# Kernel tuning notes

Hardware: AMD Instinct MI355X
Metric: run time of the kernel (lower is better)

The kernel has to match this reference:

```python
import jax, jax.numpy as jnp
import numpy as np

B, W, F, H = 2048, 64, 128, 128


def setup_inputs() -> dict:
    key = jax.random.key(0)
    ks = jax.random.split(key, 23)
    n = lambda k, shape: jax.random.normal(k, shape, dtype=jnp.float32) * 0.05
    return dict(
        X=jax.random.normal(ks[0], (B, W, F), dtype=jnp.float32),
        # InputAttention: linear1 (W+2H -> W), linear2 (W -> 1)
        ia_W1=n(ks[1], (W, W + 2 * H)), ia_b1=n(ks[2], (W,)),
        ia_W2=n(ks[3], (1, W)), ia_b2=n(ks[4], (1,)),
        # encoder LSTMCell(F, H)
        enc_Wih=n(ks[5], (4 * H, F)), enc_Whh=n(ks[6], (4 * H, H)),
        enc_bih=n(ks[7], (4 * H,)), enc_bhh=n(ks[8], (4 * H,)),
        # TemporalAttention: linear1 (3H -> H), linear2 (H -> 1)
        ta_W1=n(ks[9], (H, 3 * H)), ta_b1=n(ks[10], (H,)),
        ta_W2=n(ks[11], (1, H)), ta_b2=n(ks[12], (1,)),
        # decoder LSTMCell(1, H)
        dec_Wih=n(ks[13], (4 * H, 1)), dec_Whh=n(ks[14], (4 * H, H)),
        dec_bih=n(ks[15], (4 * H,)), dec_bhh=n(ks[16], (4 * H,)),
        # output heads
        l1_W=n(ks[17], (1, 1 + H)), l1_b=n(ks[18], (1,)),
        l2_W=n(ks[19], (H, 2 * H)), l2_b=n(ks[20], (H,)),
        l3_W=n(ks[21], (1, H)), l3_b=n(ks[22], (1,)),
    )


def _lstm_cell(x, h, c, Wih, Whh, bih, bhh):
    g = x @ Wih.T + bih + h @ Whh.T + bhh
    i, f, gg, o = jnp.split(g, 4, axis=-1)
    c_new = jax.nn.sigmoid(f) * c + jax.nn.sigmoid(i) * jnp.tanh(gg)
    h_new = jax.nn.sigmoid(o) * jnp.tanh(c_new)
    return h_new, c_new


def reference(X, ia_W1, ia_b1, ia_W2, ia_b2,
              enc_Wih, enc_Whh, enc_bih, enc_bhh,
              ta_W1, ta_b1, ta_W2, ta_b2,
              dec_Wih, dec_Whh, dec_bih, dec_bhh,
              l1_W, l1_b, l2_W, l2_b, l3_W, l3_b):
    Bsz, Wlen, Fdim = X.shape
    Hdim = enc_Whh.shape[1]
    Xf = jnp.transpose(X, (2, 0, 1))  # [F, B, W] (feature-major view for input attention)

    # ---- encoder with input attention ----
    def enc_step(carry, xt):  # xt: [B, F]
        h, c = carry
        hr = jnp.broadcast_to(h[None], (Fdim, Bsz, Hdim))
        cr = jnp.broadcast_to(c[None], (Fdim, Bsz, Hdim))
        u = jnp.tanh(jnp.concatenate([Xf, hr, cr], axis=-1) @ ia_W1.T + ia_b1)  # [F,B,W]
        e = u @ ia_W2.T + ia_b2                                                  # [F,B,1]
        alpha = jax.nn.softmax(e, axis=0)[..., 0].T                              # [B,F]
        h_new, c_new = _lstm_cell(alpha * xt, h, c, enc_Wih, enc_Whh, enc_bih, enc_bhh)
        return (h_new, c_new), h_new

    z = jnp.zeros((Bsz, Hdim), dtype=X.dtype)
    (_, _), Hs = jax.lax.scan(enc_step, (z, z), jnp.transpose(X, (1, 0, 2)))  # Hs: [W,B,H]
    # dropout: eval mode (identity)

    # ---- decoder with temporal attention ----
    def dec_step(carry, _):
        d, ds, out = carry
        dr = jnp.broadcast_to(d[None], Hs.shape)
        dsr = jnp.broadcast_to(ds[None], Hs.shape)
        v = jnp.tanh(jnp.concatenate([Hs, dr, dsr], axis=-1) @ ta_W1.T + ta_b1)  # [W,B,H]
        l = v @ ta_W2.T + ta_b2                                                   # [W,B,1]
        beta = jax.nn.softmax(l, axis=0)
        ct = jnp.sum(beta * Hs, axis=0)                                           # [B,H]
        yt = jnp.concatenate([out, ct], axis=-1) @ l1_W.T + l1_b                  # [B,1]
        d_new, ds_new = _lstm_cell(yt, d, ds, dec_Wih, dec_Whh, dec_bih, dec_bhh)
        o = jnp.concatenate([ct, d_new], axis=-1) @ l2_W.T + l2_b
        out_new = jax.nn.sigmoid(o @ l3_W.T + l3_b)                               # [B,1]
        return (d_new, ds_new, out_new), None

    out0 = jnp.zeros((Bsz, 1), dtype=X.dtype)
    (_, _, output), _ = jax.lax.scan(dec_step, (z, z, out0), None, length=Wlen)
    return output
```

## Files before the change

kernel.cpp:

```cpp
#include <hip/hip_runtime.h>
#include <hip/hip_fp16.h>
#include <stdint.h>

typedef unsigned int uint;
typedef unsigned short ushort;

#define NB 2048
#define NW 64
#define NF 128
#define NH 128

typedef __attribute__((ext_vector_type(8))) short s8v;
typedef __attribute__((ext_vector_type(8))) _Float16 h8v;
typedef __attribute__((ext_vector_type(4))) float f4v;

#define MFMA16(a, b, c) __builtin_amdgcn_mfma_f32_16x16x32_bf16((a), (b), (c), 0, 0, 0)
#define MFMAH(a, b, c)  __builtin_amdgcn_mfma_f32_16x16x32_f16((a), (b), (c), 0, 0, 0)

union H8 { h8v v; __half2 h2[4]; uint4 u4; ushort us[8]; };

__device__ __forceinline__ float bfl(uint u){ return __uint_as_float(u << 16); }
__device__ __forceinline__ float bfh(uint u){ return __uint_as_float(u & 0xffff0000u); }
__device__ __forceinline__ ushort f2bf(float f){
  uint u = __float_as_uint(f);
  u += 0x7fffu + ((u >> 16) & 1u);
  return (ushort)(u >> 16);
}
__device__ __forceinline__ float bf2f(ushort s){ return __uint_as_float(((uint)s) << 16); }

__device__ __forceinline__ float fast_tanh(float x){
  float e = __expf(x + x);
  return 1.f - 2.f * __builtin_amdgcn_rcpf(e + 1.f);
}
__device__ __forceinline__ float fast_sig(float x){
  return __builtin_amdgcn_rcpf(1.f + __expf(-x));
}
__device__ __forceinline__ ushort expo_h(float x){
  return __half_as_ushort(__float2half(__expf(x + x)));
}

__device__ __forceinline__ s8v packW(const float* p){
  s8v r;
  #pragma unroll
  for (int i = 0; i < 8; ++i) r[i] = (short)f2bf(p[i]);
  return r;
}

__global__ __launch_bounds__(256) void k_upre(const float* __restrict__ X,
                                              const float* __restrict__ iaW1,
                                              ushort* __restrict__ Eenc){
  __shared__ __align__(16) float sXT[128*68];
  const int tid = threadIdx.x, lane = tid & 63, wave = tid >> 6, g = lane >> 4;
  int b = blockIdx.x;
  const float* Xb = X + (size_t)b*NW*NF;
  for (int i = tid; i < NW*NF; i += 256){
    int j = i >> 7, f = i & 127;
    sXT[f*68 + j] = Xb[i];
  }
  s8v bw[2];
  {
    int w = wave*16 + (lane & 15);
    #pragma unroll
    for (int kb = 0; kb < 2; ++kb) bw[kb] = packW(iaW1 + w*320 + kb*32 + g*8);
  }
  __syncthreads();
  ushort* outb = Eenc + (size_t)b*NF*NW;
  int w = wave*16 + (lane & 15);
  #pragma unroll
  for (int mt = 0; mt < 8; ++mt){
    int f = mt*16 + (lane & 15);
    f4v acc = {0.f,0.f,0.f,0.f};
    #pragma unroll
    for (int kb = 0; kb < 2; ++kb){
      const float* p = &sXT[f*68 + kb*32 + g*8];
      s8v a;
      #pragma unroll
      for (int i = 0; i < 8; ++i) a[i] = (short)f2bf(p[i]);
      acc = MFMA16(a, bw[kb], acc);
    }
    int fr = mt*16 + g*4;
    #pragma unroll
    for (int j = 0; j < 4; ++j) outb[(fr + j)*64 + w] = expo_h(acc[j]);
  }
}

__global__ __launch_bounds__(256) void k_vpre(const ushort* __restrict__ Hsb,
                                              const float* __restrict__ taW1,
                                              ushort* __restrict__ Edec,
                                              ushort* __restrict__ HsT){
  __shared__ __align__(16) ushort sH[64*136];
  const int tid = threadIdx.x, lane = tid & 63, wave = tid >> 6, g = lane >> 4;
  int b = blockIdx.x;
  const ushort* Hb = Hsb + (size_t)b*NW*NH;
  for (int i = tid; i < 1024; i += 256){
    int w = i >> 4, c = i & 15;
    *(uint4*)&sH[w*136 + c*8] = *(const uint4*)(Hb + i*8);
  }
  s8v bw[2][4];
  #pragma unroll
  for (int nt = 0; nt < 2; ++nt){
    int h = wave*32 + nt*16 + (lane & 15);
    #pragma unroll
    for (int kb = 0; kb < 4; ++kb)
      bw[nt][kb] = packW(taW1 + h*384 + kb*32 + g*8);
  }
  __syncthreads();
  ushort* ho = HsT + (size_t)b*NH*NW;
  for (int k = 0; k < 32; ++k){
    int i2 = tid + 256*k;
    int h = i2 >> 6, w2 = i2 & 63;
    ho[i2] = sH[w2*136 + h];
  }
  ushort* outb = Edec + (size_t)b*NW*NH;
  #pragma unroll
  for (int mt = 0; mt < 4; ++mt){
    s8v af[4];
    #pragma unroll
    for (int kb = 0; kb < 4; ++kb)
      af[kb] = *(const s8v*)&sH[(mt*16 + (lane&15))*136 + kb*32 + g*8];
    #pragma unroll
    for (int nt = 0; nt < 2; ++nt){
      f4v acc = {0.f,0.f,0.f,0.f};
      #pragma unroll
      for (int kb = 0; kb < 4; ++kb) acc = MFMA16(af[kb], bw[nt][kb], acc);
      int h = wave*32 + nt*16 + (lane&15);
      int wr = mt*16 + g*4;
      #pragma unroll
      for (int j = 0; j < 4; ++j) outb[(wr + j)*128 + h] = expo_h(acc[j]);
    }
  }
}

__global__ __launch_bounds__(512, 2) void k_enc(
    const float* __restrict__ X, const float* __restrict__ iaW1,
    const float* __restrict__ iab1, const float* __restrict__ iaW2,
    const float* __restrict__ encWih, const float* __restrict__ encWhh,
    const float* __restrict__ encbih, const float* __restrict__ encbhh,
    const ushort* __restrict__ Eenc, ushort* __restrict__ Hsb){
  __shared__ __align__(16) ushort sUp[65536];
  __shared__ __align__(16) ushort sAB[16*264];
  __shared__ __align__(16) ushort uhc_h[8*64];
  __shared__ __align__(16) float  c_s[8*128];
  __shared__ __align__(16) float  bias_s[512];
  __shared__ __align__(16) float  xrow[8*128];

  const int tid = threadIdx.x, lane = tid & 63, wave = tid >> 6, g = lane >> 4;
  const int bbase = blockIdx.x * 8;

  for (int i = tid; i < 16*264; i += 512) sAB[i] = 0;
  for (int i = tid; i < 1024; i += 512) c_s[i] = 0.f;
  bias_s[tid] = encbih[tid] + encbhh[tid];
  {
    const ushort* up0 = Eenc + (size_t)bbase*NF*NW;
    #pragma unroll
    for (int k = 0; k < 16; ++k){
      int c = tid + k*512;
      int f = (c >> 3) & 127, s = c & 7;
      uint4 v = *(const uint4*)(up0 + (size_t)c*8);
      *(uint4*)((char*)sUp + (c>>3)*128 + ((s ^ (f & 7)) << 4)) = v;
    }
  }
  s8v bwC[4][8];
  #pragma unroll
  for (int gg = 0; gg < 4; ++gg){
    int j = gg*128 + wave*16 + (lane & 15);
    #pragma unroll
    for (int kc = 0; kc < 8; ++kc){
      const float* p = (kc < 4) ? (encWih + j*128 + kc*32) : (encWhh + j*128 + (kc-4)*32);
      bwC[gg][kc] = packW(p + g*8);
    }
  }
  s8v bwA[8];
  if (wave < 4){
    int n = wave*16 + (lane & 15);
    #pragma unroll
    for (int kc = 0; kc < 8; ++kc){
      int col = (kc < 4) ? (192 + kc*32) : (64 + (kc-4)*32);
      bwA[kc] = packW(iaW1 + n*320 + col + g*8);
    }
  }
  H8 w2f[2];
  #pragma unroll
  for (int kb = 0; kb < 2; ++kb)
    #pragma unroll
    for (int i = 0; i < 8; ++i)
      w2f[kb].v[i] = (_Float16)iaW2[kb*32 + g*8 + i];
  __syncthreads();

  for (int t = 0; t < NW; ++t){
    {
      const float* Xr = X + ((size_t)(bbase + wave)*NW + t)*NF;
      xrow[wave*128 + lane] = Xr[lane];
      xrow[wave*128 + 64 + lane] = Xr[64 + lane];
    }
    s8v aT[8];
    #pragma unroll
    for (int kc = 0; kc < 8; ++kc)
      aT[kc] = *(const s8v*)((const char*)sAB + (lane&15)*528 + kc*64 + g*16);
    if (wave < 4){
      f4v acc = {0.f,0.f,0.f,0.f};
      #pragma unroll
      for (int kc = 0; kc < 8; ++kc) acc = MFMA16(aT[kc], bwA[kc], acc);
      if (lane < 32){
        int n = wave*16 + (lane & 15);
        float b1v = iab1[n];
        int mb = g*4;
        #pragma unroll
        for (int j = 0; j < 4; ++j) uhc_h[(mb+j)*64 + n] = expo_h(acc[j] + b1v);
      }
    }
    __syncthreads();

    {
      int bb = wave;
      const char* Eb = (const char*)sUp + bb*16384;
      H8 sv[2];
      #pragma unroll
      for (int kb = 0; kb < 2; ++kb)
        sv[kb].u4 = *(const uint4*)((const char*)uhc_h + bb*128 + kb*64 + g*16);
      __half2 one2 = __float2half2_rn(1.f);
      f4v Mc[8];
      #pragma unroll
      for (int ft = 0; ft < 8; ++ft){
        int f = ft*16 + (lane & 15);
        const char* rowp = Eb + f*128;
        f4v acc = {0.f,0.f,0.f,0.f};
        #pragma unroll
        for (int kb = 0; kb < 2; ++kb){
          H8 e, a;
          e.v = *(const h8v*)(rowp + (((kb*4 + g) ^ (f & 7)) << 4));
          #pragma unroll
          for (int q = 0; q < 4; ++q) a.h2[q] = h2rcp(__hfma2(e.h2[q], sv[kb].h2[q], one2));
          acc = MFMAH(a.v, w2f[kb].v, acc);
        }
        Mc[ft] = acc;
      }
      float mn = Mc[0][0];
      #pragma unroll
      for (int ft = 0; ft < 8; ++ft)
        #pragma unroll
        for (int r = 0; r < 4; ++r) mn = fminf(mn, Mc[ft][r]);
      mn = fminf(mn, __shfl_xor(mn, 16, 64));
      mn = fminf(mn, __shfl_xor(mn, 32, 64));
      float xs[8][4]; float ssum = 0.f;
      #pragma unroll
      for (int ft = 0; ft < 8; ++ft)
        #pragma unroll
        for (int r = 0; r < 4; ++r){ float x = __expf(2.f*(mn - Mc[ft][r])); xs[ft][r] = x; ssum += x; }
      ssum += __shfl_xor(ssum, 16, 64);
      ssum += __shfl_xor(ssum, 32, 64);
      float inv = __builtin_amdgcn_rcpf(ssum);
      if ((lane & 15) == 0){
        #pragma unroll
        for (int ft = 0; ft < 8; ++ft){
          int f0 = ft*16 + g*4;
          float4 Xv = *(const float4*)&xrow[bb*128 + f0];
          uint lo = (uint)f2bf(xs[ft][0]*inv*Xv.x) | ((uint)f2bf(xs[ft][1]*inv*Xv.y) << 16);
          uint hi = (uint)f2bf(xs[ft][2]*inv*Xv.z) | ((uint)f2bf(xs[ft][3]*inv*Xv.w) << 16);
          *(uint2*)((char*)sAB + bb*528 + f0*2) = make_uint2(lo, hi);
        }
      }
    }
    __syncthreads();

    s8v aX[4];
    #pragma unroll
    for (int kc = 0; kc < 4; ++kc)
      aX[kc] = *(const s8v*)((const char*)sAB + (lane&15)*528 + kc*64 + g*16);
    __syncthreads();

    {
      f4v acc[4];
      #pragma unroll
      for (int gg = 0; gg < 4; ++gg) acc[gg] = (f4v){0.f,0.f,0.f,0.f};
      #pragma unroll
      for (int kc = 0; kc < 8; ++kc){
        s8v af = (kc < 4) ? aX[kc] : aT[kc];
        #pragma unroll
        for (int gg = 0; gg < 4; ++gg) acc[gg] = MFMA16(af, bwC[gg][kc], acc[gg]);
      }
      if (lane < 32){
        int n16 = wave*16 + (lane & 15);
        int mb = g*4;
        float bi = bias_s[n16], bf_ = bias_s[128+n16], bg = bias_s[256+n16], bo = bias_s[384+n16];
        #pragma unroll
        for (int j = 0; j < 4; ++j){
          int m = mb + j;
          float gi = acc[0][j] + bi;
          float gf = acc[1][j] + bf_;
          float gg2 = acc[2][j] + bg;
          float go = acc[3][j] + bo;
          float cold = c_s[m*128 + n16];
          float cn = fast_sig(gf)*cold + fast_sig(gi)*fast_tanh(gg2);
          float hn = fast_sig(go)*fast_tanh(cn);
          c_s[m*128 + n16] = cn;
          sAB[m*264 + n16] = f2bf(cn);
          sAB[m*264 + 128 + n16] = f2bf(hn);
          Hsb[((size_t)(bbase + m)*NW + t)*NH + n16] = f2bf(hn);
        }
      }
    }
    __syncthreads();
  }
}

__global__ __launch_bounds__(512, 2) void k_dec(
    const float* __restrict__ taW1, const float* __restrict__ tab1,
    const float* __restrict__ taW2,
    const float* __restrict__ decWih, const float* __restrict__ decWhh,
    const float* __restrict__ decbih, const float* __restrict__ decbhh,
    const float* __restrict__ l1W, const float* __restrict__ l1b,
    const float* __restrict__ l2W, const float* __restrict__ l2b,
    const float* __restrict__ l3W, const float* __restrict__ l3b,
    const ushort* __restrict__ Edec, const ushort* __restrict__ HsT,
    float* __restrict__ out){
  __shared__ __align__(16) ushort sVp[65536];
  __shared__ __align__(16) ushort sAB[16*264];
  __shared__ __align__(16) ushort sCT[16*136];
  __shared__ __align__(16) ushort vd_h[8*128];
  __shared__ __align__(16) ushort lb_bf[8*64];
  __shared__ __align__(16) ushort sW2h[128];
  __shared__ __align__(16) float  o_s[8*128];
  __shared__ __align__(16) float  cds_s[1024];
  __shared__ __align__(16) float  bias_s[512];
  __shared__ __align__(16) float  wih_s[512];
  __shared__ float yt_s[8], out_s[8];

  const int tid = threadIdx.x, lane = tid & 63, wave = tid >> 6, g = lane >> 4;
  const int bbase = blockIdx.x * 8;

  for (int i = tid; i < 16*264; i += 512) sAB[i] = 0;
  for (int i = tid; i < 16*136; i += 512) sCT[i] = 0;
  for (int i = tid; i < 1024; i += 512) cds_s[i] = 0.f;
  bias_s[tid] = decbih[tid] + decbhh[tid];
  wih_s[tid] = decWih[tid];
  if (tid < 128) sW2h[tid] = __half_as_ushort(__float2half(taW2[tid]));
  if (tid < 8) out_s[tid] = 0.f;
  {
    const ushort* vp0 = Edec + (size_t)bbase*NW*NH;
    #pragma unroll
    for (int k = 0; k < 16; ++k){
      int c = tid + k*512;
      int w = (c >> 4) & 63, s = c & 15;
      uint4 v = *(const uint4*)(vp0 + (size_t)c*8);
      *(uint4*)((char*)sVp + (c >> 4)*256 + ((s ^ (w & 15)) << 4)) = v;
    }
  }
  s8v bwA[8];
  {
    int n = wave*16 + (lane & 15);
    #pragma unroll
    for (int kc = 0; kc < 8; ++kc)
      bwA[kc] = packW(taW1 + n*384 + 128 + kc*32 + g*8);
  }
  s8v bwD[4][4];
  #pragma unroll
  for (int gg = 0; gg < 4; ++gg){
    int j = gg*128 + wave*16 + (lane & 15);
    #pragma unroll
    for (int kc = 0; kc < 4; ++kc)
      bwD[gg][kc] = packW(decWhh + j*128 + kc*32 + g*8);
  }
  s8v bwF[8];
  {
    int n = wave*16 + (lane & 15);
    #pragma unroll
    for (int kc = 0; kc < 8; ++kc)
      bwF[kc] = packW(l2W + n*256 + kc*32 + g*8);
  }
  float l1w[8];
  #pragma unroll
  for (int ht = 0; ht < 8; ++ht) l1w[ht] = l1W[1 + ht*16 + (lane & 15)];
  __syncthreads();

  for (int t = 0; t < NW; ++t){
    s8v aT[8];
    #pragma unroll
    for (int kc = 0; kc < 8; ++kc)
      aT[kc] = *(const s8v*)((const char*)sAB + (lane&15)*528 + kc*64 + g*16);
    {
      f4v acc = {0.f,0.f,0.f,0.f};
      #pragma unroll
      for (int kc = 0; kc < 8; ++kc) acc = MFMA16(aT[kc], bwA[kc], acc);
      if (lane < 32){
        int n = wave*16 + (lane & 15);
        float tb = tab1[n];
        int mb = g*4;
        #pragma unroll
        for (int j = 0; j < 4; ++j) vd_h[(mb+j)*128 + n] = expo_h(acc[j] + tb);
      }
    }
    __syncthreads();

    {
      int bb = wave;
      const ushort* hb = HsT + (size_t)(bbase + bb)*NH*NW;
      s8v hbf[8][2];
      #pragma unroll
      for (int ht = 0; ht < 8; ++ht){
        int h = ht*16 + (lane & 15);
        #pragma unroll
        for (int kb = 0; kb < 2; ++kb)
          hbf[ht][kb] = *(const s8v*)(hb + h*64 + kb*32 + g*8);
      }
      const char* Eb = (const char*)sVp + bb*16384;
      H8 sv[4];
      #pragma unroll
      for (int kb = 0; kb < 4; ++kb)
        sv[kb].u4 = *(const uint4*)((const char*)vd_h + bb*256 + kb*64 + g*16);
      __half2 one2 = __float2half2_rn(1.f);
      f4v Mc[4];
      #pragma unroll
      for (int wt = 0; wt < 4; ++wt){
        int w = wt*16 + (lane & 15);
        const char* rowp = Eb + w*256;
        f4v acc = {0.f,0.f,0.f,0.f};
        #pragma unroll
        for (int kb = 0; kb < 4; ++kb){
          H8 e, a, wv;
          wv.u4 = *(const uint4*)&sW2h[kb*32 + g*8];
          e.v = *(const h8v*)(rowp + (((kb*4 + g) ^ (w & 15)) << 4));
          #pragma unroll
          for (int q = 0; q < 4; ++q) a.h2[q] = h2rcp(__hfma2(e.h2[q], sv[kb].h2[q], one2));
          acc = MFMAH(a.v, wv.v, acc);
        }
        Mc[wt] = acc;
      }
      float mn = Mc[0][0];
      #pragma unroll
      for (int wt = 0; wt < 4; ++wt)
        #pragma unroll
        for (int r = 0; r < 4; ++r) mn = fminf(mn, Mc[wt][r]);
      mn = fminf(mn, __shfl_xor(mn, 16, 64));
      mn = fminf(mn, __shfl_xor(mn, 32, 64));
      float xs[4][4]; float ssum = 0.f;
      #pragma unroll
      for (int wt = 0; wt < 4; ++wt)
        #pragma unroll
        for (int r = 0; r < 4; ++r){ float x = __expf(2.f*(mn - Mc[wt][r])); xs[wt][r] = x; ssum += x; }
      ssum += __shfl_xor(ssum, 16, 64);
      ssum += __shfl_xor(ssum, 32, 64);
      float inv = __builtin_amdgcn_rcpf(ssum);
      if ((lane & 15) == 0){
        #pragma unroll
        for (int wt = 0; wt < 4; ++wt){
          int w0 = wt*16 + g*4;
          uint lo = (uint)f2bf(xs[wt][0]*inv) | ((uint)f2bf(xs[wt][1]*inv) << 16);
          uint hi = (uint)f2bf(xs[wt][2]*inv) | ((uint)f2bf(xs[wt][3]*inv) << 16);
          *(uint2*)((char*)lb_bf + bb*128 + w0*2) = make_uint2(lo, hi);
        }
      }
      s8v ba[2];
      #pragma unroll
      for (int kb = 0; kb < 2; ++kb)
        ba[kb] = *(const s8v*)((const char*)lb_bf + bb*128 + kb*64 + g*16);
      float p = 0.f;
      #pragma unroll
      for (int ht = 0; ht < 8; ++ht){
        f4v acc = {0.f,0.f,0.f,0.f};
        #pragma unroll
        for (int kb = 0; kb < 2; ++kb) acc = MFMA16(ba[kb], hbf[ht][kb], acc);
        float ctv = acc[0];
        if (lane < 16) sCT[bb*136 + ht*16 + (lane&15)] = f2bf(ctv);
        p += l1w[ht] * ctv;
      }
      p += __shfl_xor(p, 1, 64);
      p += __shfl_xor(p, 2, 64);
      p += __shfl_xor(p, 4, 64);
      p += __shfl_xor(p, 8, 64);
      if (lane == 0) yt_s[bb] = p + l1W[0]*out_s[bb] + l1b[0];
    }
    __syncthreads();

    {
      f4v g4[4];
      #pragma unroll
      for (int gg = 0; gg < 4; ++gg) g4[gg] = (f4v){0.f,0.f,0.f,0.f};
      #pragma unroll
      for (int kc = 0; kc < 4; ++kc){
        #pragma unroll
        for (int gg = 0; gg < 4; ++gg) g4[gg] = MFMA16(aT[kc], bwD[gg][kc], g4[gg]);
      }
      if (lane < 32){
        int n16 = wave*16 + (lane & 15);
        int mb = g*4;
        float bi = bias_s[n16], bf_ = bias_s[128+n16], bg = bias_s[256+n16], bo = bias_s[384+n16];
        float wi = wih_s[n16], wf = wih_s[128+n16], wg = wih_s[256+n16], wo = wih_s[384+n16];
        #pragma unroll
        for (int j = 0; j < 4; ++j){
          int m = mb + j;
          float yt = yt_s[m];
          float gi = g4[0][j] + bi + wi*yt;
          float gf = g4[1][j] + bf_ + wf*yt;
          float gg2 = g4[2][j] + bg + wg*yt;
          float go = g4[3][j] + bo + wo*yt;
          float cold = cds_s[m*128 + n16];
          float cn = fast_sig(gf)*cold + fast_sig(gi)*fast_tanh(gg2);
          float hn = fast_sig(go)*fast_tanh(cn);
          cds_s[m*128 + n16] = cn;
          sAB[m*264 + n16] = f2bf(hn);
          sAB[m*264 + 128 + n16] = f2bf(cn);
        }
      }
    }
    __syncthreads();

    {
      f4v of = {0.f,0.f,0.f,0.f};
      #pragma unroll
      for (int kc = 0; kc < 4; ++kc){
        s8v af = *(const s8v*)((const char*)sCT + (lane&15)*272 + kc*64 + g*16);
        of = MFMA16(af, bwF[kc], of);
      }
      #pragma unroll
      for (int kc = 4; kc < 8; ++kc){
        s8v af = *(const s8v*)((const char*)sAB + (lane&15)*528 + (kc-4)*64 + g*16);
        of = MFMA16(af, bwF[kc], of);
      }
      if (lane < 32){
        int n16 = wave*16 + (lane & 15);
        int mb = g*4;
        float l2bv = l2b[n16];
        #pragma unroll
        for (int j = 0; j < 4; ++j) o_s[(mb + j)*128 + n16] = of[j] + l2bv;
      }
    }
    __syncthreads();

    {
      int bb = wave;
      float o0 = o_s[bb*128 + 2*lane], o1 = o_s[bb*128 + 2*lane + 1];
      float p = l3W[2*lane]*o0 + l3W[2*lane + 1]*o1;
      #pragma unroll
      for (int off = 32; off; off >>= 1) p += __shfl_xor(p, off, 64);
      if (lane == 0) out_s[bb] = fast_sig(p + l3b[0]);
    }
  }
  __syncthreads();
  if (tid < 8) out[bbase + tid] = out_s[tid];
}

extern "C" void kernel_launch(void* const* d_in, const int* in_sizes, int n_in,
                              void* d_out, int out_size, void* d_ws, size_t ws_size,
                              hipStream_t stream){
  const float* X      = (const float*)d_in[0];
  const float* iaW1   = (const float*)d_in[1];
  const float* iab1   = (const float*)d_in[2];
  const float* iaW2   = (const float*)d_in[3];
  const float* encWih = (const float*)d_in[5];
  const float* encWhh = (const float*)d_in[6];
  const float* encbih = (const float*)d_in[7];
  const float* encbhh = (const float*)d_in[8];
  const float* taW1   = (const float*)d_in[9];
  const float* tab1   = (const float*)d_in[10];
  const float* taW2   = (const float*)d_in[11];
  const float* decWih = (const float*)d_in[13];
  const float* decWhh = (const float*)d_in[14];
  const float* decbih = (const float*)d_in[15];
  const float* decbhh = (const float*)d_in[16];
  const float* l1W    = (const float*)d_in[17];
  const float* l1b    = (const float*)d_in[18];
  const float* l2W    = (const float*)d_in[19];
  const float* l2b    = (const float*)d_in[20];
  const float* l3W    = (const float*)d_in[21];
  const float* l3b    = (const float*)d_in[22];

  char* ws = (char*)d_ws;
  ushort* Eenc = (ushort*)(ws);
  ushort* Hsb  = (ushort*)(ws + 33554432);
  ushort* HsT  = (ushort*)(ws + 2*33554432);
  ushort* Edec = Eenc;

  k_upre<<<dim3(2048), dim3(256), 0, stream>>>(X, iaW1, Eenc);
  k_enc<<<dim3(256), dim3(512), 0, stream>>>(X, iaW1, iab1, iaW2,
                                             encWih, encWhh, encbih, encbhh,
                                             Eenc, Hsb);
  k_vpre<<<dim3(2048), dim3(256), 0, stream>>>(Hsb, taW1, Edec, HsT);
  k_dec<<<dim3(256), dim3(512), 0, stream>>>(taW1, tab1, taW2,
                                             decWih, decWhh, decbih, decbhh,
                                             l1W, l1b, l2W, l2b, l3W, l3b,
                                             Edec, HsT, (float*)d_out);
}
```

Baseline: 1.161 ms.

## Keep LSTM state and biases in registers, fuse output head reduction, drop softmax max

Moves the cell state, gate biases and small weights from shared memory into per-thread registers in both the encoder and decoder kernels. In the decoder, the l2/l3 output projection is reduced in-register per wave and written as partial sums. The sigmoid for the previous output is folded into the next step's gate computation, which removes one barrier-separated phase per step. It also drops the max-subtraction in both softmaxes, which relies on the attention logits being bounded (tanh-based) to avoid overflow. The cost is higher register pressure, which could hurt occupancy at the existing 512-thread launch bound.

```diff
diff --git a/kernel.cpp b/kernel.cpp
--- a/kernel.cpp
+++ b/kernel.cpp
@@ -140,16 +140,13 @@
   __shared__ __align__(16) ushort sUp[65536];
   __shared__ __align__(16) ushort sAB[16*264];
   __shared__ __align__(16) ushort uhc_h[8*64];
-  __shared__ __align__(16) float  c_s[8*128];
-  __shared__ __align__(16) float  bias_s[512];
   __shared__ __align__(16) float  xrow[8*128];
 
   const int tid = threadIdx.x, lane = tid & 63, wave = tid >> 6, g = lane >> 4;
   const int bbase = blockIdx.x * 8;
+  const int n16 = wave*16 + (lane & 15);
 
   for (int i = tid; i < 16*264; i += 512) sAB[i] = 0;
-  for (int i = tid; i < 1024; i += 512) c_s[i] = 0.f;
-  bias_s[tid] = encbih[tid] + encbhh[tid];
   {
     const ushort* up0 = Eenc + (size_t)bbase*NF*NW;
     #pragma unroll
@@ -160,10 +157,16 @@
       *(uint4*)((char*)sUp + (c>>3)*128 + ((s ^ (f & 7)) << 4)) = v;
     }
   }
+  float bias_r[4];
+  #pragma unroll
+  for (int gg = 0; gg < 4; ++gg)
+    bias_r[gg] = encbih[gg*128 + n16] + encbhh[gg*128 + n16];
+  float b1_r = iab1[n16 & 63];
+  float c_r[4] = {0.f, 0.f, 0.f, 0.f};
   s8v bwC[4][8];
   #pragma unroll
   for (int gg = 0; gg < 4; ++gg){
-    int j = gg*128 + wave*16 + (lane & 15);
+    int j = gg*128 + n16;
     #pragma unroll
     for (int kc = 0; kc < 8; ++kc){
       const float* p = (kc < 4) ? (encWih + j*128 + kc*32) : (encWhh + j*128 + (kc-4)*32);
@@ -172,11 +175,10 @@
   }
   s8v bwA[8];
   if (wave < 4){
-    int n = wave*16 + (lane & 15);
     #pragma unroll
     for (int kc = 0; kc < 8; ++kc){
       int col = (kc < 4) ? (192 + kc*32) : (64 + (kc-4)*32);
-      bwA[kc] = packW(iaW1 + n*320 + col + g*8);
+      bwA[kc] = packW(iaW1 + n16*320 + col + g*8);
     }
   }
   H8 w2f[2];
@@ -202,11 +204,9 @@
       #pragma unroll
       for (int kc = 0; kc < 8; ++kc) acc = MFMA16(aT[kc], bwA[kc], acc);
       if (lane < 32){
-        int n = wave*16 + (lane & 15);
-        float b1v = iab1[n];
         int mb = g*4;
         #pragma unroll
-        for (int j = 0; j < 4; ++j) uhc_h[(mb+j)*64 + n] = expo_h(acc[j] + b1v);
+        for (int j = 0; j < 4; ++j) uhc_h[(mb+j)*64 + n16] = expo_h(acc[j] + b1_r);
       }
     }
     __syncthreads();
@@ -235,18 +235,11 @@
         }
         Mc[ft] = acc;
       }
-      float mn = Mc[0][0];
+      float xs[8][4]; float ssum = 0.f;
       #pragma unroll
       for (int ft = 0; ft < 8; ++ft)
         #pragma unroll
-        for (int r = 0; r < 4; ++r) mn = fminf(mn, Mc[ft][r]);
-      mn = fminf(mn, __shfl_xor(mn, 16, 64));
-      mn = fminf(mn, __shfl_xor(mn, 32, 64));
-      float xs[8][4]; float ssum = 0.f;
-      #pragma unroll
-      for (int ft = 0; ft < 8; ++ft)
-        #pragma unroll
-        for (int r = 0; r < 4; ++r){ float x = __expf(2.f*(mn - Mc[ft][r])); xs[ft][r] = x; ssum += x; }
+        for (int r = 0; r < 4; ++r){ float x = __expf(-2.f*Mc[ft][r]); xs[ft][r] = x; ssum += x; }
       ssum += __shfl_xor(ssum, 16, 64);
       ssum += __shfl_xor(ssum, 32, 64);
       float inv = __builtin_amdgcn_rcpf(ssum);
@@ -280,20 +273,18 @@
         for (int gg = 0; gg < 4; ++gg) acc[gg] = MFMA16(af, bwC[gg][kc], acc[gg]);
       }
       if (lane < 32){
-        int n16 = wave*16 + (lane & 15);
         int mb = g*4;
-        float bi = bias_s[n16], bf_ = bias_s[128+n16], bg = bias_s[256+n16], bo = bias_s[384+n16];
         #pragma unroll
         for (int j = 0; j < 4; ++j){
           int m = mb + j;
-          float gi = acc[0][j] + bi;
-          float gf = acc[1][j] + bf_;
-          float gg2 = acc[2][j] + bg;
-          float go = acc[3][j] + bo;
-          float cold = c_s[m*128 + n16];
+          float gi = acc[0][j] + bias_r[0];
+          float gf = acc[1][j] + bias_r[1];
+          float gg2 = acc[2][j] + bias_r[2];
+          float go = acc[3][j] + bias_r[3];
+          float cold = c_r[j];
           float cn = fast_sig(gf)*cold + fast_sig(gi)*fast_tanh(gg2);
           float hn = fast_sig(go)*fast_tanh(cn);
-          c_s[m*128 + n16] = cn;
+          c_r[j] = cn;
           sAB[m*264 + n16] = f2bf(cn);
           sAB[m*264 + 128 + n16] = f2bf(hn);
           Hsb[((size_t)(bbase + m)*NW + t)*NH + n16] = f2bf(hn);
@@ -319,23 +310,15 @@
   __shared__ __align__(16) ushort sCT[16*136];
   __shared__ __align__(16) ushort vd_h[8*128];
   __shared__ __align__(16) ushort lb_bf[8*64];
-  __shared__ __align__(16) ushort sW2h[128];
-  __shared__ __align__(16) float  o_s[8*128];
-  __shared__ __align__(16) float  cds_s[1024];
-  __shared__ __align__(16) float  bias_s[512];
-  __shared__ __align__(16) float  wih_s[512];
-  __shared__ float yt_s[8], out_s[8];
+  __shared__ __align__(16) float  op_s[8][8];
+  __shared__ __align__(16) float  yt_s[8];
 
   const int tid = threadIdx.x, lane = tid & 63, wave = tid >> 6, g = lane >> 4;
   const int bbase = blockIdx.x * 8;
+  const int n16 = wave*16 + (lane & 15);
 
   for (int i = tid; i < 16*264; i += 512) sAB[i] = 0;
   for (int i = tid; i < 16*136; i += 512) sCT[i] = 0;
-  for (int i = tid; i < 1024; i += 512) cds_s[i] = 0.f;
-  bias_s[tid] = decbih[tid] + decbhh[tid];
-  wih_s[tid] = decWih[tid];
-  if (tid < 128) sW2h[tid] = __half_as_ushort(__float2half(taW2[tid]));
-  if (tid < 8) out_s[tid] = 0.f;
   {
     const ushort* vp0 = Edec + (size_t)bbase*NW*NH;
     #pragma unroll
@@ -346,28 +329,39 @@
       *(uint4*)((char*)sVp + (c >> 4)*256 + ((s ^ (w & 15)) << 4)) = v;
     }
   }
+  float bias_r[4], wih_r[4];
+  #pragma unroll
+  for (int gg = 0; gg < 4; ++gg){
+    bias_r[gg] = decbih[gg*128 + n16] + decbhh[gg*128 + n16];
+    wih_r[gg]  = decWih[gg*128 + n16];
+  }
+  float tab1_r = tab1[n16];
+  float l2b_r  = l2b[n16];
+  float l3w_r  = l3W[n16];
+  float l1w0 = l1W[0], l1b0 = l1b[0], l3b0 = l3b[0];
+  float cds_r[4] = {0.f, 0.f, 0.f, 0.f};
   s8v bwA[8];
-  {
-    int n = wave*16 + (lane & 15);
-    #pragma unroll
-    for (int kc = 0; kc < 8; ++kc)
-      bwA[kc] = packW(taW1 + n*384 + 128 + kc*32 + g*8);
-  }
+  #pragma unroll
+  for (int kc = 0; kc < 8; ++kc)
+    bwA[kc] = packW(taW1 + n16*384 + 128 + kc*32 + g*8);
   s8v bwD[4][4];
   #pragma unroll
   for (int gg = 0; gg < 4; ++gg){
-    int j = gg*128 + wave*16 + (lane & 15);
+    int j = gg*128 + n16;
     #pragma unroll
     for (int kc = 0; kc < 4; ++kc)
       bwD[gg][kc] = packW(decWhh + j*128 + kc*32 + g*8);
   }
   s8v bwF[8];
-  {
-    int n = wave*16 + (lane & 15);
-    #pragma unroll
-    for (int kc = 0; kc < 8; ++kc)
-      bwF[kc] = packW(l2W + n*256 + kc*32 + g*8);
-  }
+  #pragma unroll
+  for (int kc = 0; kc < 8; ++kc)
+    bwF[kc] = packW(l2W + n16*256 + kc*32 + g*8);
+  H8 w2df[4];
+  #pragma unroll
+  for (int kb = 0; kb < 4; ++kb)
+    #pragma unroll
+    for (int i = 0; i < 8; ++i)
+      w2df[kb].v[i] = (_Float16)taW2[kb*32 + g*8 + i];
   float l1w[8];
   #pragma unroll
   for (int ht = 0; ht < 8; ++ht) l1w[ht] = l1W[1 + ht*16 + (lane & 15)];
@@ -383,11 +377,9 @@
       #pragma unroll
       for (int kc = 0; kc < 8; ++kc) acc = MFMA16(aT[kc], bwA[kc], acc);
       if (lane < 32){
-        int n = wave*16 + (lane & 15);
-        float tb = tab1[n];
         int mb = g*4;
         #pragma unroll
-        for (int j = 0; j < 4; ++j) vd_h[(mb+j)*128 + n] = expo_h(acc[j] + tb);
+        for (int j = 0; j < 4; ++j) vd_h[(mb+j)*128 + n16] = expo_h(acc[j] + tab1_r);
       }
     }
     __syncthreads();
@@ -417,27 +409,19 @@
         f4v acc = {0.f,0.f,0.f,0.f};
         #pragma unroll
         for (int kb = 0; kb < 4; ++kb){
-          H8 e, a, wv;
-          wv.u4 = *(const uint4*)&sW2h[kb*32 + g*8];
+          H8 e, a;
           e.v = *(const h8v*)(rowp + (((kb*4 + g) ^ (w & 15)) << 4));
           #pragma unroll
           for (int q = 0; q < 4; ++q) a.h2[q] = h2rcp(__hfma2(e.h2[q], sv[kb].h2[q], one2));
-          acc = MFMAH(a.v, wv.v, acc);
+          acc = MFMAH(a.v, w2df[kb].v, acc);
         }
         Mc[wt] = acc;
       }
-      float mn = Mc[0][0];
+      float xs[4][4]; float ssum = 0.f;
       #pragma unroll
       for (int wt = 0; wt < 4; ++wt)
         #pragma unroll
-        for (int r = 0; r < 4; ++r) mn = fminf(mn, Mc[wt][r]);
-      mn = fminf(mn, __shfl_xor(mn, 16, 64));
-      mn = fminf(mn, __shfl_xor(mn, 32, 64));
-      float xs[4][4]; float ssum = 0.f;
-      #pragma unroll
-      for (int wt = 0; wt < 4; ++wt)
-        #pragma unroll
-        for (int r = 0; r < 4; ++r){ float x = __expf(2.f*(mn - Mc[wt][r])); xs[wt][r] = x; ssum += x; }
+        for (int r = 0; r < 4; ++r){ float x = __expf(-2.f*Mc[wt][r]); xs[wt][r] = x; ssum += x; }
       ssum += __shfl_xor(ssum, 16, 64);
       ssum += __shfl_xor(ssum, 32, 64);
       float inv = __builtin_amdgcn_rcpf(ssum);
@@ -468,7 +452,7 @@
       p += __shfl_xor(p, 2, 64);
       p += __shfl_xor(p, 4, 64);
       p += __shfl_xor(p, 8, 64);
-      if (lane == 0) yt_s[bb] = p + l1W[0]*out_s[bb] + l1b[0];
+      if (lane == 0) yt_s[bb] = p + l1b0;
     }
     __syncthreads();
 
@@ -482,22 +466,27 @@
         for (int gg = 0; gg < 4; ++gg) g4[gg] = MFMA16(aT[kc], bwD[gg][kc], g4[gg]);
       }
       if (lane < 32){
-        int n16 = wave*16 + (lane & 15);
         int mb = g*4;
-        float bi = bias_s[n16], bf_ = bias_s[128+n16], bg = bias_s[256+n16], bo = bias_s[384+n16];
-        float wi = wih_s[n16], wf = wih_s[128+n16], wg = wih_s[256+n16], wo = wih_s[384+n16];
+        float4 so = make_float4(0.f, 0.f, 0.f, 0.f);
+        #pragma unroll
+        for (int w = 0; w < 8; ++w){
+          float4 v = *(const float4*)((const char*)op_s + w*32 + g*16);
+          so.x += v.x; so.y += v.y; so.z += v.z; so.w += v.w;
+        }
+        float soa[4] = {so.x, so.y, so.z, so.w};
         #pragma unroll
         for (int j = 0; j < 4; ++j){
           int m = mb + j;
-          float yt = yt_s[m];
-          float gi = g4[0][j] + bi + wi*yt;
-          float gf = g4[1][j] + bf_ + wf*yt;
-          float gg2 = g4[2][j] + bg + wg*yt;
-          float go = g4[3][j] + bo + wo*yt;
-          float cold = cds_s[m*128 + n16];
+          float outp = (t == 0) ? 0.f : fast_sig(soa[j] + l3b0);
+          float yt = yt_s[m] + l1w0*outp;
+          float gi = g4[0][j] + bias_r[0] + wih_r[0]*yt;
+          float gf = g4[1][j] + bias_r[1] + wih_r[1]*yt;
+          float gg2 = g4[2][j] + bias_r[2] + wih_r[2]*yt;
+          float go = g4[3][j] + bias_r[3] + wih_r[3]*yt;
+          float cold = cds_r[j];
           float cn = fast_sig(gf)*cold + fast_sig(gi)*fast_tanh(gg2);
           float hn = fast_sig(go)*fast_tanh(cn);
-          cds_s[m*128 + n16] = cn;
+          cds_r[j] = cn;
           sAB[m*264 + n16] = f2bf(hn);
           sAB[m*264 + 128 + n16] = f2bf(cn);
         }
@@ -517,27 +506,29 @@
         s8v af = *(const s8v*)((const char*)sAB + (lane&15)*528 + (kc-4)*64 + g*16);
         of = MFMA16(af, bwF[kc], of);
       }
-      if (lane < 32){
-        int n16 = wave*16 + (lane & 15);
-        int mb = g*4;
-        float l2bv = l2b[n16];
-        #pragma unroll
-        for (int j = 0; j < 4; ++j) o_s[(mb + j)*128 + n16] = of[j] + l2bv;
-      }
-    }
-    __syncthreads();
-
-    {
-      int bb = wave;
-      float o0 = o_s[bb*128 + 2*lane], o1 = o_s[bb*128 + 2*lane + 1];
-      float p = l3W[2*lane]*o0 + l3W[2*lane + 1]*o1;
-      #pragma unroll
-      for (int off = 32; off; off >>= 1) p += __shfl_xor(p, off, 64);
-      if (lane == 0) out_s[bb] = fast_sig(p + l3b[0]);
+      float p0 = l3w_r*(of[0] + l2b_r);
+      float p1 = l3w_r*(of[1] + l2b_r);
+      float p2 = l3w_r*(of[2] + l2b_r);
+      float p3 = l3w_r*(of[3] + l2b_r);
+      #pragma unroll
+      for (int off = 1; off <= 8; off <<= 1){
+        p0 += __shfl_xor(p0, off, 64);
+        p1 += __shfl_xor(p1, off, 64);
+        p2 += __shfl_xor(p2, off, 64);
+        p3 += __shfl_xor(p3, off, 64);
+      }
+      if ((lane & 15) == 0 && lane < 32){
+        *(float4*)((char*)op_s + wave*32 + g*16) = make_float4(p0, p1, p2, p3);
+      }
     }
   }
   __syncthreads();
-  if (tid < 8) out[bbase + tid] = out_s[tid];
+  if (tid < 8){
+    float s = 0.f;
+    #pragma unroll
+    for (int w = 0; w < 8; ++w) s += op_s[w][tid];
+    out[bbase + tid] = fast_sig(s + l3b0);
+  }
 }
 
 extern "C" void kernel_launch(void* const* d_in, const int* in_sizes, int n_in,
```

Result: no change. 1.153 ms (-0.7%).
